# Optimization experiments

Measured on AMD Instinct MI355X. Metric: run time of the kernel, lower is better.

The kernel has to match this reference:

```python
import jax, jax.numpy as jnp
import numpy as np

N_NODES = 100000


def _gcn_propagate(x, src, dst, n):
    """Symmetric-normalized propagation with self-loops (PyG gcn_norm, K=1).

    out[dst] += deg^-1/2[src] * deg^-1/2[dst] * x[src], including self-loops.
    """
    loop = jnp.arange(n, dtype=src.dtype)
    s = jnp.concatenate([src, loop])
    d = jnp.concatenate([dst, loop])
    deg = jax.ops.segment_sum(jnp.ones_like(d, dtype=x.dtype), d, num_segments=n)
    dinv = jnp.where(deg > 0, jax.lax.rsqrt(deg), jnp.zeros_like(deg))
    norm = dinv[s] * dinv[d]            # [E+N]
    msg = x[s] * norm[:, None]          # [E+N, F] gathered messages
    return jax.ops.segment_sum(msg, d, num_segments=n)


def setup_inputs() -> dict:
    key = jax.random.key(0)
    ks = jax.random.split(key, 6)
    n, e, f, h, c = N_NODES, 1600000, 64, 64, 16
    x = jax.random.normal(ks[0], (n, f), dtype=jnp.float32)
    edge_index = jax.random.randint(ks[1], (2, e), 0, n, dtype=jnp.int64)
    W1 = jax.random.normal(ks[2], (h, f), dtype=jnp.float32) * 0.1
    b1 = jnp.zeros((h,), dtype=jnp.float32)
    W2 = jax.random.normal(ks[3], (h, h), dtype=jnp.float32) * 0.1
    b2 = jnp.zeros((h,), dtype=jnp.float32)
    W3 = jax.random.normal(ks[4], (c, h), dtype=jnp.float32) * 0.1
    b3 = jnp.zeros((c,), dtype=jnp.float32)
    return {"x": x, "edge_index": edge_index, "W1": W1, "b1": b1,
            "W2": W2, "b2": b2, "W3": W3, "b3": b3}


def reference(x, edge_index, W1, b1, W2, b2, W3, b3):
    n = x.shape[0]
    src, dst = edge_index[0], edge_index[1]
    # SGConv 1 (K=1): propagate then linear; dropout is identity in eval mode
    h = _gcn_propagate(x, src, dst, n) @ W1.T + b1
    h = jax.nn.relu(h)
    # SGConv 2
    h = _gcn_propagate(h, src, dst, n) @ W2.T + b2
    h = jax.nn.relu(h)
    # final linear
    return h @ W3.T + b3
```

## Files before the change

### kernel.cpp

```cpp
#include <hip/hip_runtime.h>
#include <hip/hip_fp16.h>


#define F 64
#define C 16
#define SCAN_B 1024

__device__ __forceinline__ float rl(float v, int l) {
    return __uint_as_float(__builtin_amdgcn_readlane(__float_as_uint(v), l));
}

__device__ __forceinline__ float4 ld_h4(const float2* base, size_t idx) {
    float2 raw = base[idx];
    __half2 lo = __builtin_bit_cast(__half2, raw.x);
    __half2 hi = __builtin_bit_cast(__half2, raw.y);
    float2 f0 = __half22float2(lo);
    float2 f1 = __half22float2(hi);
    return make_float4(f0.x, f0.y, f1.x, f1.y);
}

__device__ __forceinline__ float2 ld_h2(const unsigned int* base, size_t idx) {
    unsigned int raw = base[idx];
    return __half22float2(__builtin_bit_cast(__half2, raw));
}

__global__ void degrank_kernel(const int* __restrict__ dst, int* __restrict__ deg,
                               int* __restrict__ rank, int E) {
    int i = (blockIdx.x * blockDim.x + threadIdx.x) * 4;
    if (i + 4 <= E) {
        int4 d = *(const int4*)(dst + i);
        rank[i]     = atomicAdd(&deg[d.x], 1);
        rank[i + 1] = atomicAdd(&deg[d.y], 1);
        rank[i + 2] = atomicAdd(&deg[d.z], 1);
        rank[i + 3] = atomicAdd(&deg[d.w], 1);
    } else {
        for (int k = i; k < E; ++k) rank[k] = atomicAdd(&deg[dst[k]], 1);
    }
}

__global__ __launch_bounds__(256) void scan1_kernel(const int* __restrict__ deg,
                                                    int* __restrict__ part,
                                                    int* __restrict__ bsum, int n) {
    __shared__ int ts[256];
    int b = blockIdx.x, t = threadIdx.x;
    int base = b * SCAN_B + t * 4;
    int v[4], sum = 0;
#pragma unroll
    for (int k = 0; k < 4; ++k) { int i = base + k; v[k] = (i < n) ? deg[i] : 0; sum += v[k]; }
    ts[t] = sum;
    __syncthreads();
    for (int off = 1; off < 256; off <<= 1) {
        int add = (t >= off) ? ts[t - off] : 0;
        __syncthreads();
        ts[t] += add;
        __syncthreads();
    }
    int run = ts[t] - sum;
#pragma unroll
    for (int k = 0; k < 4; ++k) { int i = base + k; if (i < n) part[i] = run; run += v[k]; }
    if (t == 255) bsum[b] = ts[255];
}

__global__ __launch_bounds__(256) void scan2_kernel(int* __restrict__ bsum, int nb) {
    __shared__ int ts[256];
    int t = threadIdx.x;
    int v = (t < nb) ? bsum[t] : 0;
    ts[t] = v;
    __syncthreads();
    for (int off = 1; off < 256; off <<= 1) {
        int add = (t >= off) ? ts[t - off] : 0;
        __syncthreads();
        ts[t] += add;
        __syncthreads();
    }
    if (t < nb) bsum[t] = ts[t] - v;
}

__global__ void scan3_kernel(const int* __restrict__ part, const int* __restrict__ bsum,
                             const int* __restrict__ deg, int* __restrict__ rowptr,
                             float* __restrict__ dinv, int n, int E) {
    int i = blockIdx.x * blockDim.x + threadIdx.x;
    if (i < n) {
        rowptr[i] = part[i] + bsum[i / SCAN_B];
        dinv[i] = rsqrtf((float)deg[i] + 1.0f);
    }
    if (i == 0) rowptr[n] = E;
}

__global__ void fill_kernel(const int* __restrict__ src, const int* __restrict__ dst,
                            const int* __restrict__ rank, const int* __restrict__ rowptr,
                            int* __restrict__ csr_src, int E) {
    int i = (blockIdx.x * blockDim.x + threadIdx.x) * 4;
    if (i + 4 <= E) {
        int4 s = *(const int4*)(src + i);
        int4 d = *(const int4*)(dst + i);
        int4 r = *(const int4*)(rank + i);
        csr_src[rowptr[d.x] + r.x] = s.x;
        csr_src[rowptr[d.y] + r.y] = s.y;
        csr_src[rowptr[d.z] + r.z] = s.z;
        csr_src[rowptr[d.w] + r.w] = s.w;
    } else {
        for (int k = i; k < E; ++k) csr_src[rowptr[dst[k]] + rank[k]] = src[k];
    }
}

__global__ __launch_bounds__(256) void gemm1_kernel(
    const float4* __restrict__ in4, const float* __restrict__ W,
    const float* __restrict__ scale, __half* __restrict__ yout, int n) {
    int tid = threadIdx.x;
    int lane = tid & 63;
    int m = lane & 15;
    float4 w[16];
#pragma unroll
    for (int t = 0; t < 16; ++t) w[t] = *(const float4*)(W + (size_t)lane * F + 4 * t);
    int gw = blockIdx.x * 4 + (tid >> 6);
    int nw = gridDim.x * 4;
    int node = gw;
    if (node >= n) return;
    float4 v = in4[(size_t)node * 16 + m];
    while (true) {
        int nxt = node + nw;
        float4 vn;
        if (nxt < n) vn = in4[(size_t)nxt * 16 + m];
        float acc = 0.0f;
#pragma unroll
        for (int t = 0; t < 16; ++t) {
            acc = fmaf(rl(v.x, t), w[t].x, acc);
            acc = fmaf(rl(v.y, t), w[t].y, acc);
            acc = fmaf(rl(v.z, t), w[t].z, acc);
            acc = fmaf(rl(v.w, t), w[t].w, acc);
        }
        acc *= scale[node];
        yout[(size_t)node * F + lane] = __float2half(acc);
        if (nxt >= n) break;
        v = vn;
        node = nxt;
    }
}

__global__ __launch_bounds__(256) void gemm2_kernel(
    const float2* __restrict__ in2, const float* __restrict__ W,
    __half* __restrict__ yout, int n) {
    int tid = threadIdx.x;
    int lane = tid & 63;
    int m = lane & 15;
    float4 w[16];
#pragma unroll
    for (int t = 0; t < 16; ++t) w[t] = *(const float4*)(W + (size_t)lane * F + 4 * t);
    int gw = blockIdx.x * 4 + (tid >> 6);
    int nw = gridDim.x * 4;
    int node = gw;
    if (node >= n) return;
    float4 v = ld_h4(in2, (size_t)node * 16 + m);
    while (true) {
        int nxt = node + nw;
        float4 vn;
        if (nxt < n) vn = ld_h4(in2, (size_t)nxt * 16 + m);
        float acc = 0.0f;
#pragma unroll
        for (int t = 0; t < 16; ++t) {
            acc = fmaf(rl(v.x, t), w[t].x, acc);
            acc = fmaf(rl(v.y, t), w[t].y, acc);
            acc = fmaf(rl(v.z, t), w[t].z, acc);
            acc = fmaf(rl(v.w, t), w[t].w, acc);
        }
        yout[(size_t)node * F + lane] = __float2half(acc);
        if (nxt >= n) break;
        v = vn;
        node = nxt;
    }
}

__global__ __launch_bounds__(256) void gather1_kernel(
    const unsigned int* __restrict__ y, const int* __restrict__ rowptr,
    const int* __restrict__ csr_src, const float* __restrict__ dinv,
    const float* __restrict__ b1, unsigned int* __restrict__ h1s, int n) {
    int tid = threadIdx.x;
    int m = tid & 15;
    int s = blockIdx.x & 1;
    int g = blockIdx.x >> 1;
    int fo = 16 * s + m;
    float2 bias = *(const float2*)(b1 + 32 * s + 2 * m);
    int qid = g * 16 + (tid >> 4);
    int nq = (gridDim.x >> 1) << 4;
    for (int node = qid; node < n; node += nq) {
        int beg = rowptr[node], end = rowptr[node + 1];
        float2 a0 = {0, 0}, a1 = {0, 0}, a2 = {0, 0}, a3 = {0, 0};
        int p = beg;
        for (; p + 8 <= end; p += 8) {
            int s0 = csr_src[p],     s1 = csr_src[p + 1];
            int s2 = csr_src[p + 2], s3 = csr_src[p + 3];
            int s4 = csr_src[p + 4], s5 = csr_src[p + 5];
            int s6 = csr_src[p + 6], s7 = csr_src[p + 7];
            float2 v0 = ld_h2(y, (size_t)s0 * 32 + fo);
            float2 v1 = ld_h2(y, (size_t)s1 * 32 + fo);
            float2 v2 = ld_h2(y, (size_t)s2 * 32 + fo);
            float2 v3 = ld_h2(y, (size_t)s3 * 32 + fo);
            float2 v4 = ld_h2(y, (size_t)s4 * 32 + fo);
            float2 v5 = ld_h2(y, (size_t)s5 * 32 + fo);
            float2 v6 = ld_h2(y, (size_t)s6 * 32 + fo);
            float2 v7 = ld_h2(y, (size_t)s7 * 32 + fo);
            a0.x += v0.x + v4.x; a0.y += v0.y + v4.y;
            a1.x += v1.x + v5.x; a1.y += v1.y + v5.y;
            a2.x += v2.x + v6.x; a2.y += v2.y + v6.y;
            a3.x += v3.x + v7.x; a3.y += v3.y + v7.y;
        }
        if (p + 4 <= end) {
            int s0 = csr_src[p], s1 = csr_src[p + 1], s2 = csr_src[p + 2], s3 = csr_src[p + 3];
            float2 v0 = ld_h2(y, (size_t)s0 * 32 + fo);
            float2 v1 = ld_h2(y, (size_t)s1 * 32 + fo);
            float2 v2 = ld_h2(y, (size_t)s2 * 32 + fo);
            float2 v3 = ld_h2(y, (size_t)s3 * 32 + fo);
            a0.x += v0.x; a0.y += v0.y;
            a1.x += v1.x; a1.y += v1.y;
            a2.x += v2.x; a2.y += v2.y;
            a3.x += v3.x; a3.y += v3.y;
            p += 4;
        }
        for (; p < end; ++p) {
            int sv = csr_src[p];
            float2 v = ld_h2(y, (size_t)sv * 32 + fo);
            a0.x += v.x; a0.y += v.y;
        }
        a0.x += a1.x + a2.x + a3.x;
        a0.y += a1.y + a2.y + a3.y;
        float dd = dinv[node];
        float2 self = ld_h2(y, (size_t)node * 32 + fo);
        float2 r;
        r.x = dd * fmaxf(fmaf(dd, a0.x + self.x, bias.x), 0.0f);
        r.y = dd * fmaxf(fmaf(dd, a0.y + self.y, bias.y), 0.0f);
        h1s[(size_t)node * 32 + fo] =
            __builtin_bit_cast(unsigned int, __float22half2_rn(make_float2(r.x, r.y)));
    }
}

__global__ __launch_bounds__(256) void gather2_kernel(
    const float2* __restrict__ y, const int* __restrict__ rowptr,
    const int* __restrict__ csr_src, const float* __restrict__ dinv,
    const float* __restrict__ b2, const float* __restrict__ W3,
    const float* __restrict__ b3, float* __restrict__ out, int n) {
    int tid = threadIdx.x;
    int lane = tid & 63;
    int m = lane & 15;
    int qbase = lane & 48;
    float4 bias = *(const float4*)(b2 + 4 * m);
    float b3r = b3[m];
    int qid = (blockIdx.x * 256 + tid) >> 4;
    int nq = (gridDim.x * 256) >> 4;
    for (int node = qid; node < n; node += nq) {
        int beg = rowptr[node], end = rowptr[node + 1];
        float4 a0 = {0, 0, 0, 0}, a1 = {0, 0, 0, 0}, a2 = {0, 0, 0, 0}, a3 = {0, 0, 0, 0};
        int p = beg;
        for (; p + 8 <= end; p += 8) {
            int s0 = csr_src[p],     s1 = csr_src[p + 1];
            int s2 = csr_src[p + 2], s3 = csr_src[p + 3];
            int s4 = csr_src[p + 4], s5 = csr_src[p + 5];
            int s6 = csr_src[p + 6], s7 = csr_src[p + 7];
            float4 v0 = ld_h4(y, (size_t)s0 * 16 + m);
            float4 v1 = ld_h4(y, (size_t)s1 * 16 + m);
            float4 v2 = ld_h4(y, (size_t)s2 * 16 + m);
            float4 v3 = ld_h4(y, (size_t)s3 * 16 + m);
            float4 v4 = ld_h4(y, (size_t)s4 * 16 + m);
            float4 v5 = ld_h4(y, (size_t)s5 * 16 + m);
            float4 v6 = ld_h4(y, (size_t)s6 * 16 + m);
            float4 v7 = ld_h4(y, (size_t)s7 * 16 + m);
            a0.x += v0.x + v4.x; a0.y += v0.y + v4.y; a0.z += v0.z + v4.z; a0.w += v0.w + v4.w;
            a1.x += v1.x + v5.x; a1.y += v1.y + v5.y; a1.z += v1.z + v5.z; a1.w += v1.w + v5.w;
            a2.x += v2.x + v6.x; a2.y += v2.y + v6.y; a2.z += v2.z + v6.z; a2.w += v2.w + v6.w;
            a3.x += v3.x + v7.x; a3.y += v3.y + v7.y; a3.z += v3.z + v7.z; a3.w += v3.w + v7.w;
        }
        if (p + 4 <= end) {
            int s0 = csr_src[p], s1 = csr_src[p + 1], s2 = csr_src[p + 2], s3 = csr_src[p + 3];
            float4 v0 = ld_h4(y, (size_t)s0 * 16 + m);
            float4 v1 = ld_h4(y, (size_t)s1 * 16 + m);
            float4 v2 = ld_h4(y, (size_t)s2 * 16 + m);
            float4 v3 = ld_h4(y, (size_t)s3 * 16 + m);
            a0.x += v0.x; a0.y += v0.y; a0.z += v0.z; a0.w += v0.w;
            a1.x += v1.x; a1.y += v1.y; a1.z += v1.z; a1.w += v1.w;
            a2.x += v2.x; a2.y += v2.y; a2.z += v2.z; a2.w += v2.w;
            a3.x += v3.x; a3.y += v3.y; a3.z += v3.z; a3.w += v3.w;
            p += 4;
        }
        for (; p < end; ++p) {
            int s = csr_src[p];
            float4 v = ld_h4(y, (size_t)s * 16 + m);
            a0.x += v.x; a0.y += v.y; a0.z += v.z; a0.w += v.w;
        }
        a0.x += a1.x + a2.x + a3.x;
        a0.y += a1.y + a2.y + a3.y;
        a0.z += a1.z + a2.z + a3.z;
        a0.w += a1.w + a2.w + a3.w;
        float dd = dinv[node];
        float4 self = ld_h4(y, (size_t)node * 16 + m);
        float4 h;
        h.x = fmaxf(fmaf(dd, a0.x + self.x, bias.x), 0.0f);
        h.y = fmaxf(fmaf(dd, a0.y + self.y, bias.y), 0.0f);
        h.z = fmaxf(fmaf(dd, a0.z + self.z, bias.z), 0.0f);
        h.w = fmaxf(fmaf(dd, a0.w + self.w, bias.w), 0.0f);
        float acc = 0.0f;
#pragma unroll
        for (int t = 0; t < 16; ++t) {
            float4 wv = *(const float4*)(W3 + (size_t)m * F + 4 * t);
            float hx = __shfl(h.x, qbase + t);
            float hy = __shfl(h.y, qbase + t);
            float hz = __shfl(h.z, qbase + t);
            float hw = __shfl(h.w, qbase + t);
            acc = fmaf(hx, wv.x, fmaf(hy, wv.y, fmaf(hz, wv.z, fmaf(hw, wv.w, acc))));
        }
        out[(size_t)node * C + m] = acc + b3r;
    }
}

extern "C" void kernel_launch(void* const* d_in, const int* in_sizes, int n_in,
                              void* d_out, int out_size, void* d_ws, size_t ws_size,
                              hipStream_t stream) {
    const float* x  = (const float*)d_in[0];
    const int* edge = (const int*)d_in[1];
    const float* W1 = (const float*)d_in[2];
    const float* b1 = (const float*)d_in[3];
    const float* W2 = (const float*)d_in[4];
    const float* b2 = (const float*)d_in[5];
    const float* W3 = (const float*)d_in[6];
    const float* b3 = (const float*)d_in[7];
    float* out = (float*)d_out;

    int n = in_sizes[0] / F;
    int E = in_sizes[1] / 2;
    const int* src = edge;
    const int* dst = edge + E;

    int nb = (n + SCAN_B - 1) / SCAN_B;

    char* ws = (char*)d_ws;
    size_t o = 0;
    auto alloc = [&](size_t bytes) { char* p = ws + o; o += (bytes + 255) & ~(size_t)255; return p; };
    int*    deg     = (int*)   alloc((size_t)n * 4);
    int*    rank    = (int*)   alloc((size_t)E * 4);
    int*    part    = (int*)   alloc((size_t)n * 4);
    int*    bsum    = (int*)   alloc(256 * 4);
    int*    rowptr  = (int*)   alloc((size_t)(n + 1) * 4);
    int*    csr_src = (int*)   alloc((size_t)E * 4);
    float*  dinv    = (float*) alloc((size_t)n * 4);
    __half* y1      = (__half*)alloc((size_t)n * F * 2);
    __half* h1s     = (__half*)alloc((size_t)n * F * 2);
    __half* y2      = y1;

    hipMemsetAsync(deg, 0, (size_t)n * 4, stream);
    degrank_kernel<<<(E / 4 + 255) / 256, 256, 0, stream>>>(dst, deg, rank, E);

    scan1_kernel<<<nb, 256, 0, stream>>>(deg, part, bsum, n);
    scan2_kernel<<<1, 256, 0, stream>>>(bsum, nb);
    scan3_kernel<<<(n + 255) / 256, 256, 0, stream>>>(part, bsum, deg, rowptr, dinv, n, E);

    gemm1_kernel<<<2048, 256, 0, stream>>>((const float4*)x, W1, dinv, y1, n);

    fill_kernel<<<(E / 4 + 255) / 256, 256, 0, stream>>>(src, dst, rank, rowptr, csr_src, E);

    gather1_kernel<<<2048, 256, 0, stream>>>(
        (const unsigned int*)y1, rowptr, csr_src, dinv, b1, (unsigned int*)h1s, n);

    gemm2_kernel<<<2048, 256, 0, stream>>>((const float2*)h1s, W2, y2, n);

    gather2_kernel<<<2048, 256, 0, stream>>>(
        (const float2*)y2, rowptr, csr_src, dinv, b2, W3, b3, out, n);
}
```

Measured before the change: 310.0 us.

## Split feature tables into 16-column slabs and gather per slab

The intermediate feature tables move from row-major [n,64] half to four column slabs of [n,16] halves. Each gather block now works on one slab, so the random-access working set per pass is a quarter of the table and more likely to stay in cache. The two gather kernels become one templated kernel using 8-byte loads and nontemporal loads/stores for the index stream and outputs. The final 64->16 linear is split into its own lin3 kernel, which adds a launch and a full pass over h2 in exchange for a simpler gather.

```diff
diff --git a/kernel.cpp b/kernel.cpp
--- a/kernel.cpp
+++ b/kernel.cpp
@@ -10,18 +10,24 @@
     return __uint_as_float(__builtin_amdgcn_readlane(__float_as_uint(v), l));
 }
 
-__device__ __forceinline__ float4 ld_h4(const float2* base, size_t idx) {
-    float2 raw = base[idx];
-    __half2 lo = __builtin_bit_cast(__half2, raw.x);
-    __half2 hi = __builtin_bit_cast(__half2, raw.y);
+__device__ __forceinline__ float4 unpack_h4(unsigned long long raw) {
+    __half2 lo = __builtin_bit_cast(__half2, (unsigned int)(raw & 0xffffffffull));
+    __half2 hi = __builtin_bit_cast(__half2, (unsigned int)(raw >> 32));
     float2 f0 = __half22float2(lo);
     float2 f1 = __half22float2(hi);
     return make_float4(f0.x, f0.y, f1.x, f1.y);
 }
-
-__device__ __forceinline__ float2 ld_h2(const unsigned int* base, size_t idx) {
-    unsigned int raw = base[idx];
-    return __half22float2(__builtin_bit_cast(__half2, raw));
+__device__ __forceinline__ float4 ld_h4_nt(const unsigned long long* base, size_t idx) {
+    return unpack_h4(__builtin_nontemporal_load(base + idx));
+}
+__device__ __forceinline__ float4 ld_h4_c(const unsigned long long* base, size_t idx) {
+    return unpack_h4(base[idx]);
+}
+__device__ __forceinline__ unsigned long long pack_h4(float4 r) {
+    __half2 lo = __float22half2_rn(make_float2(r.x, r.y));
+    __half2 hi = __float22half2_rn(make_float2(r.z, r.w));
+    return (unsigned long long)__builtin_bit_cast(unsigned int, lo) |
+           ((unsigned long long)__builtin_bit_cast(unsigned int, hi) << 32);
 }
 
 __global__ void degrank_kernel(const int* __restrict__ dst, int* __restrict__ deg,
@@ -113,6 +119,7 @@
     float4 w[16];
 #pragma unroll
     for (int t = 0; t < 16; ++t) w[t] = *(const float4*)(W + (size_t)lane * F + 4 * t);
+    __half* outp = yout + (size_t)(lane >> 4) * n * 16 + (lane & 15);
     int gw = blockIdx.x * 4 + (tid >> 6);
     int nw = gridDim.x * 4;
     int node = gw;
@@ -131,7 +138,7 @@
             acc = fmaf(rl(v.w, t), w[t].w, acc);
         }
         acc *= scale[node];
-        yout[(size_t)node * F + lane] = __float2half(acc);
+        outp[(size_t)node * 16] = __float2half(acc);
         if (nxt >= n) break;
         v = vn;
         node = nxt;
@@ -139,7 +146,7 @@
 }
 
 __global__ __launch_bounds__(256) void gemm2_kernel(
-    const float2* __restrict__ in2, const float* __restrict__ W,
+    const unsigned long long* __restrict__ intab, const float* __restrict__ W,
     __half* __restrict__ yout, int n) {
     int tid = threadIdx.x;
     int lane = tid & 63;
@@ -147,15 +154,17 @@
     float4 w[16];
 #pragma unroll
     for (int t = 0; t < 16; ++t) w[t] = *(const float4*)(W + (size_t)lane * F + 4 * t);
+    const unsigned long long* inp = intab + (size_t)(m >> 2) * n * 4 + (m & 3);
+    __half* outp = yout + (size_t)(lane >> 4) * n * 16 + (lane & 15);
     int gw = blockIdx.x * 4 + (tid >> 6);
     int nw = gridDim.x * 4;
     int node = gw;
     if (node >= n) return;
-    float4 v = ld_h4(in2, (size_t)node * 16 + m);
+    float4 v = unpack_h4(inp[(size_t)node * 4]);
     while (true) {
         int nxt = node + nw;
         float4 vn;
-        if (nxt < n) vn = ld_h4(in2, (size_t)nxt * 16 + m);
+        if (nxt < n) vn = unpack_h4(inp[(size_t)nxt * 4]);
         float acc = 0.0f;
 #pragma unroll
         for (int t = 0; t < 16; ++t) {
@@ -164,139 +173,74 @@
             acc = fmaf(rl(v.z, t), w[t].z, acc);
             acc = fmaf(rl(v.w, t), w[t].w, acc);
         }
-        yout[(size_t)node * F + lane] = __float2half(acc);
+        outp[(size_t)node * 16] = __float2half(acc);
         if (nxt >= n) break;
         v = vn;
         node = nxt;
     }
 }
 
-__global__ __launch_bounds__(256) void gather1_kernel(
-    const unsigned int* __restrict__ y, const int* __restrict__ rowptr,
+template <bool SCALE_OUT>
+__global__ __launch_bounds__(256) void gatherS_kernel(
+    const unsigned long long* __restrict__ ytab, const int* __restrict__ rowptr,
     const int* __restrict__ csr_src, const float* __restrict__ dinv,
-    const float* __restrict__ b1, unsigned int* __restrict__ h1s, int n) {
+    const float* __restrict__ bias, unsigned long long* __restrict__ otab, int n) {
     int tid = threadIdx.x;
-    int m = tid & 15;
-    int s = blockIdx.x & 1;
-    int g = blockIdx.x >> 1;
-    int fo = 16 * s + m;
-    float2 bias = *(const float2*)(b1 + 32 * s + 2 * m);
-    int qid = g * 16 + (tid >> 4);
-    int nq = (gridDim.x >> 1) << 4;
-    for (int node = qid; node < n; node += nq) {
+    int o = tid & 3;
+    int g = tid >> 2;
+    int s = blockIdx.x & 3;
+    const unsigned long long* ys = ytab + (size_t)s * n * 4;
+    unsigned long long* os = otab + (size_t)s * n * 4;
+    float4 bb = *(const float4*)(bias + 16 * s + 4 * o);
+    int node0 = (blockIdx.x >> 2) * 64 + g;
+    int stride = (gridDim.x >> 2) * 64;
+    for (int node = node0; node < n; node += stride) {
         int beg = rowptr[node], end = rowptr[node + 1];
-        float2 a0 = {0, 0}, a1 = {0, 0}, a2 = {0, 0}, a3 = {0, 0};
+        float4 a0 = {0, 0, 0, 0}, a1 = {0, 0, 0, 0};
         int p = beg;
-        for (; p + 8 <= end; p += 8) {
-            int s0 = csr_src[p],     s1 = csr_src[p + 1];
-            int s2 = csr_src[p + 2], s3 = csr_src[p + 3];
-            int s4 = csr_src[p + 4], s5 = csr_src[p + 5];
-            int s6 = csr_src[p + 6], s7 = csr_src[p + 7];
-            float2 v0 = ld_h2(y, (size_t)s0 * 32 + fo);
-            float2 v1 = ld_h2(y, (size_t)s1 * 32 + fo);
-            float2 v2 = ld_h2(y, (size_t)s2 * 32 + fo);
-            float2 v3 = ld_h2(y, (size_t)s3 * 32 + fo);
-            float2 v4 = ld_h2(y, (size_t)s4 * 32 + fo);
-            float2 v5 = ld_h2(y, (size_t)s5 * 32 + fo);
-            float2 v6 = ld_h2(y, (size_t)s6 * 32 + fo);
-            float2 v7 = ld_h2(y, (size_t)s7 * 32 + fo);
-            a0.x += v0.x + v4.x; a0.y += v0.y + v4.y;
-            a1.x += v1.x + v5.x; a1.y += v1.y + v5.y;
-            a2.x += v2.x + v6.x; a2.y += v2.y + v6.y;
-            a3.x += v3.x + v7.x; a3.y += v3.y + v7.y;
-        }
-        if (p + 4 <= end) {
-            int s0 = csr_src[p], s1 = csr_src[p + 1], s2 = csr_src[p + 2], s3 = csr_src[p + 3];
-            float2 v0 = ld_h2(y, (size_t)s0 * 32 + fo);
-            float2 v1 = ld_h2(y, (size_t)s1 * 32 + fo);
-            float2 v2 = ld_h2(y, (size_t)s2 * 32 + fo);
-            float2 v3 = ld_h2(y, (size_t)s3 * 32 + fo);
-            a0.x += v0.x; a0.y += v0.y;
-            a1.x += v1.x; a1.y += v1.y;
-            a2.x += v2.x; a2.y += v2.y;
-            a3.x += v3.x; a3.y += v3.y;
-            p += 4;
+        for (; p + 4 <= end; p += 4) {
+            int s0 = __builtin_nontemporal_load(csr_src + p);
+            int s1 = __builtin_nontemporal_load(csr_src + p + 1);
+            int s2 = __builtin_nontemporal_load(csr_src + p + 2);
+            int s3 = __builtin_nontemporal_load(csr_src + p + 3);
+            float4 v0 = ld_h4_c(ys, (size_t)s0 * 4 + o);
+            float4 v1 = ld_h4_c(ys, (size_t)s1 * 4 + o);
+            float4 v2 = ld_h4_c(ys, (size_t)s2 * 4 + o);
+            float4 v3 = ld_h4_c(ys, (size_t)s3 * 4 + o);
+            a0.x += v0.x + v2.x; a0.y += v0.y + v2.y; a0.z += v0.z + v2.z; a0.w += v0.w + v2.w;
+            a1.x += v1.x + v3.x; a1.y += v1.y + v3.y; a1.z += v1.z + v3.z; a1.w += v1.w + v3.w;
         }
         for (; p < end; ++p) {
-            int sv = csr_src[p];
-            float2 v = ld_h2(y, (size_t)sv * 32 + fo);
-            a0.x += v.x; a0.y += v.y;
-        }
-        a0.x += a1.x + a2.x + a3.x;
-        a0.y += a1.y + a2.y + a3.y;
+            int sv = __builtin_nontemporal_load(csr_src + p);
+            float4 v = ld_h4_c(ys, (size_t)sv * 4 + o);
+            a0.x += v.x; a0.y += v.y; a0.z += v.z; a0.w += v.w;
+        }
+        a0.x += a1.x; a0.y += a1.y; a0.z += a1.z; a0.w += a1.w;
         float dd = dinv[node];
-        float2 self = ld_h2(y, (size_t)node * 32 + fo);
-        float2 r;
-        r.x = dd * fmaxf(fmaf(dd, a0.x + self.x, bias.x), 0.0f);
-        r.y = dd * fmaxf(fmaf(dd, a0.y + self.y, bias.y), 0.0f);
-        h1s[(size_t)node * 32 + fo] =
-            __builtin_bit_cast(unsigned int, __float22half2_rn(make_float2(r.x, r.y)));
-    }
-}
-
-__global__ __launch_bounds__(256) void gather2_kernel(
-    const float2* __restrict__ y, const int* __restrict__ rowptr,
-    const int* __restrict__ csr_src, const float* __restrict__ dinv,
-    const float* __restrict__ b2, const float* __restrict__ W3,
+        float4 self = ld_h4_c(ys, (size_t)node * 4 + o);
+        float4 r;
+        r.x = fmaxf(fmaf(dd, a0.x + self.x, bb.x), 0.0f);
+        r.y = fmaxf(fmaf(dd, a0.y + self.y, bb.y), 0.0f);
+        r.z = fmaxf(fmaf(dd, a0.z + self.z, bb.z), 0.0f);
+        r.w = fmaxf(fmaf(dd, a0.w + self.w, bb.w), 0.0f);
+        if (SCALE_OUT) { r.x *= dd; r.y *= dd; r.z *= dd; r.w *= dd; }
+        __builtin_nontemporal_store(pack_h4(r), os + (size_t)node * 4 + o);
+    }
+}
+
+__global__ __launch_bounds__(256) void lin3_kernel(
+    const unsigned long long* __restrict__ h2tab, const float* __restrict__ W3,
     const float* __restrict__ b3, float* __restrict__ out, int n) {
     int tid = threadIdx.x;
     int lane = tid & 63;
     int m = lane & 15;
     int qbase = lane & 48;
-    float4 bias = *(const float4*)(b2 + 4 * m);
+    const unsigned long long* inp = h2tab + (size_t)(m >> 2) * n * 4 + (m & 3);
     float b3r = b3[m];
     int qid = (blockIdx.x * 256 + tid) >> 4;
     int nq = (gridDim.x * 256) >> 4;
     for (int node = qid; node < n; node += nq) {
-        int beg = rowptr[node], end = rowptr[node + 1];
-        float4 a0 = {0, 0, 0, 0}, a1 = {0, 0, 0, 0}, a2 = {0, 0, 0, 0}, a3 = {0, 0, 0, 0};
-        int p = beg;
-        for (; p + 8 <= end; p += 8) {
-            int s0 = csr_src[p],     s1 = csr_src[p + 1];
-            int s2 = csr_src[p + 2], s3 = csr_src[p + 3];
-            int s4 = csr_src[p + 4], s5 = csr_src[p + 5];
-            int s6 = csr_src[p + 6], s7 = csr_src[p + 7];
-            float4 v0 = ld_h4(y, (size_t)s0 * 16 + m);
-            float4 v1 = ld_h4(y, (size_t)s1 * 16 + m);
-            float4 v2 = ld_h4(y, (size_t)s2 * 16 + m);
-            float4 v3 = ld_h4(y, (size_t)s3 * 16 + m);
-            float4 v4 = ld_h4(y, (size_t)s4 * 16 + m);
-            float4 v5 = ld_h4(y, (size_t)s5 * 16 + m);
-            float4 v6 = ld_h4(y, (size_t)s6 * 16 + m);
-            float4 v7 = ld_h4(y, (size_t)s7 * 16 + m);
-            a0.x += v0.x + v4.x; a0.y += v0.y + v4.y; a0.z += v0.z + v4.z; a0.w += v0.w + v4.w;
-            a1.x += v1.x + v5.x; a1.y += v1.y + v5.y; a1.z += v1.z + v5.z; a1.w += v1.w + v5.w;
-            a2.x += v2.x + v6.x; a2.y += v2.y + v6.y; a2.z += v2.z + v6.z; a2.w += v2.w + v6.w;
-            a3.x += v3.x + v7.x; a3.y += v3.y + v7.y; a3.z += v3.z + v7.z; a3.w += v3.w + v7.w;
-        }
-        if (p + 4 <= end) {
-            int s0 = csr_src[p], s1 = csr_src[p + 1], s2 = csr_src[p + 2], s3 = csr_src[p + 3];
-            float4 v0 = ld_h4(y, (size_t)s0 * 16 + m);
-            float4 v1 = ld_h4(y, (size_t)s1 * 16 + m);
-            float4 v2 = ld_h4(y, (size_t)s2 * 16 + m);
-            float4 v3 = ld_h4(y, (size_t)s3 * 16 + m);
-            a0.x += v0.x; a0.y += v0.y; a0.z += v0.z; a0.w += v0.w;
-            a1.x += v1.x; a1.y += v1.y; a1.z += v1.z; a1.w += v1.w;
-            a2.x += v2.x; a2.y += v2.y; a2.z += v2.z; a2.w += v2.w;
-            a3.x += v3.x; a3.y += v3.y; a3.z += v3.z; a3.w += v3.w;
-            p += 4;
-        }
-        for (; p < end; ++p) {
-            int s = csr_src[p];
-            float4 v = ld_h4(y, (size_t)s * 16 + m);
-            a0.x += v.x; a0.y += v.y; a0.z += v.z; a0.w += v.w;
-        }
-        a0.x += a1.x + a2.x + a3.x;
-        a0.y += a1.y + a2.y + a3.y;
-        a0.z += a1.z + a2.z + a3.z;
-        a0.w += a1.w + a2.w + a3.w;
-        float dd = dinv[node];
-        float4 self = ld_h4(y, (size_t)node * 16 + m);
-        float4 h;
-        h.x = fmaxf(fmaf(dd, a0.x + self.x, bias.x), 0.0f);
-        h.y = fmaxf(fmaf(dd, a0.y + self.y, bias.y), 0.0f);
-        h.z = fmaxf(fmaf(dd, a0.z + self.z, bias.z), 0.0f);
-        h.w = fmaxf(fmaf(dd, a0.w + self.w, bias.w), 0.0f);
+        float4 h = unpack_h4(inp[(size_t)node * 4]);
         float acc = 0.0f;
 #pragma unroll
         for (int t = 0; t < 16; ++t) {
@@ -344,6 +288,7 @@
     __half* y1      = (__half*)alloc((size_t)n * F * 2);
     __half* h1s     = (__half*)alloc((size_t)n * F * 2);
     __half* y2      = y1;
+    __half* h2      = h1s;
 
     hipMemsetAsync(deg, 0, (size_t)n * 4, stream);
     degrank_kernel<<<(E / 4 + 255) / 256, 256, 0, stream>>>(dst, deg, rank, E);
@@ -356,11 +301,17 @@
 
     fill_kernel<<<(E / 4 + 255) / 256, 256, 0, stream>>>(src, dst, rank, rowptr, csr_src, E);
 
-    gather1_kernel<<<2048, 256, 0, stream>>>(
-        (const unsigned int*)y1, rowptr, csr_src, dinv, b1, (unsigned int*)h1s, n);
-
-    gemm2_kernel<<<2048, 256, 0, stream>>>((const float2*)h1s, W2, y2, n);
-
-    gather2_kernel<<<2048, 256, 0, stream>>>(
-        (const float2*)y2, rowptr, csr_src, dinv, b2, W3, b3, out, n);
-}
+    gatherS_kernel<true><<<2048, 256, 0, stream>>>(
+        (const unsigned long long*)y1, rowptr, csr_src, dinv, b1,
+        (unsigned long long*)h1s, n);
+
+    gemm2_kernel<<<2048, 256, 0, stream>>>(
+        (const unsigned long long*)h1s, W2, y2, n);
+
+    gatherS_kernel<false><<<2048, 256, 0, stream>>>(
+        (const unsigned long long*)y2, rowptr, csr_src, dinv, b2,
+        (unsigned long long*)h2, n);
+
+    lin3_kernel<<<2048, 256, 0, stream>>>(
+        (const unsigned long long*)h2, W3, b3, out, n);
+}
```

Result: slower. 355.7 us (+14.7%).
